# Kernel tuning notes

Hardware: AMD Instinct MI355X
Metric: run time of the kernel (lower is better)

Reference implementation:

```python
import jax, jax.numpy as jnp
import numpy as np

B, D, P, E, C = 2048, 4096, 64, 8, 64
K = D // P  # conv kernel = stride = input_dim / patch_num


def setup_inputs() -> dict:
    key = jax.random.key(0)
    k1, k2, k3, k4 = jax.random.split(key, 4)
    x = jax.random.normal(k1, (B, 1, D), jnp.float32)
    router_w = jax.random.normal(k2, (E, K), jnp.float32) * 0.02   # Router conv weight [E,1,K] squeezed
    expert_w = jax.random.normal(k3, (E, 2 * C, K), jnp.float32) * 0.001  # per-expert conv weights (small=True scaling)
    expert_b = jax.random.normal(k4, (E, 2 * C), jnp.float32) * 0.001
    return {"x": x, "router_w": router_w, "expert_w": expert_w, "expert_b": expert_b}


def reference(x, router_w, expert_w, expert_b):
    b, _, d = x.shape
    e, k = router_w.shape
    p = d // k
    c = expert_w.shape[1] // 2

    # Conv1d(1, ch, K, stride=K) == per-patch matmul; sum over dim 2 == sum over patches.
    patches = x.reshape(b, p, k)                                   # [B,P,K]

    # Router (eval mode: no noise)
    select = jnp.einsum('bpk,ek->be', patches, router_w)           # [B,E]

    # top1 routing
    gate = jnp.max(select, axis=-1)                                # [B]
    index = jnp.argmax(select, axis=-1)                            # [B]
    onehot = jax.nn.one_hot(index, e, dtype=select.dtype)          # [B,E]

    # aux load-balance loss
    density = onehot.mean(axis=0)
    density_proxy = select.mean(axis=0)
    loss = (density_proxy * density).mean() * float(e ** 2)

    # combine/dispatch (mask_flat is all ones for top1)
    combine = gate[:, None] * onehot                               # [B,E]
    dispatch = jax.lax.stop_gradient((combine != 0).astype(select.dtype))  # bool cast detaches grad
    select0 = dispatch

    # Dense dispatch: every expert sees the full batch, zero-masked by dispatch.
    # z[e,b,c,p] = conv of (dispatch[b,e]*x[b]) with expert e's kernel, + bias
    z = jnp.einsum('bpk,eck->ebcp', patches, expert_w)             # [E,B,2C,P]
    z = z * dispatch.T[:, :, None, None] + expert_b[:, None, :, None]
    z = z ** 3                                                     # nonlinear=True
    s = z.sum(axis=-1)                                             # sum over patches -> [E,B,2C]
    expert_out = jnp.stack([s[..., :c].sum(-1), s[..., c:].sum(-1)], axis=-1)  # [E,B,2]

    out = jnp.einsum('be,ebl->bl', combine, expert_out)            # [B,2]
    out = jax.nn.softmax(out, axis=1)
    return out, select0, loss
```

## Files before the change

### kernel.cpp

```cpp
#include <hip/hip_runtime.h>

#define BB 2048
#define DD 4096
#define PP 64
#define KK 64
#define EE 8
#define C2 128
#define NBLK BB
#define NGRP 32

typedef __attribute__((ext_vector_type(8))) short short8;
typedef __attribute__((ext_vector_type(4))) float floatx4;

__device__ float g_sum[NGRP][16] = {};

__device__ inline unsigned pack2_trunc(float lo, float hi) {
    unsigned ul = __builtin_bit_cast(unsigned, lo);
    unsigned uh = __builtin_bit_cast(unsigned, hi);
    return (uh & 0xFFFF0000u) | (ul >> 16);
}

__device__ inline void gload16(const float* src, float* lds_dst_uniform) {
    __builtin_amdgcn_global_load_lds(
        (const __attribute__((address_space(1))) unsigned int*)src,
        (__attribute__((address_space(3))) unsigned int*)lds_dst_uniform, 16, 0, 0);
}

__global__ __launch_bounds__(256) void moe_main(
    const float* __restrict__ x, const float* __restrict__ rw,
    const float* __restrict__ ew, const float* __restrict__ eb,
    float* __restrict__ out)
{
    __shared__ float xs[64 * 64];
    __shared__ float sh_d[4][8];
    __shared__ float sh_h[4];
    const int lane = threadIdx.x & 63;
    const int w = threadIdx.x >> 6;
    const int b = blockIdx.x;
    const int r = lane & 15, q = lane >> 4;
    const float* xb = x + (size_t)b * DD;

    #pragma unroll
    for (int j = 0; j < 4; ++j) {
        const int row = w * 16 + j * 4 + (lane >> 4);
        const int g   = (lane & 15) ^ (row & 7);
        gload16(xb + row * 64 + g * 4, &xs[(w * 16 + j * 4) * 64]);
    }
    asm volatile("s_waitcnt vmcnt(0)" ::: "memory");

    const int s = r & 7;
    float ps[16];
    #pragma unroll
    for (int kb = 0; kb < 2; ++kb) {
        const float* base = &xs[(w * 16 + r) * 64 + kb * 32];
        float4 v0 = *(const float4*)(base + (((q * 2 + 0) ^ s) << 2));
        float4 v1 = *(const float4*)(base + (((q * 2 + 1) ^ s) << 2));
        ps[kb*8+0] = v0.x; ps[kb*8+1] = v0.y; ps[kb*8+2] = v0.z; ps[kb*8+3] = v0.w;
        ps[kb*8+4] = v1.x; ps[kb*8+5] = v1.y; ps[kb*8+6] = v1.z; ps[kb*8+7] = v1.w;
    }

    #pragma unroll
    for (int e2 = 0; e2 < 8; ++e2) {
        const float* rwe = rw + e2 * KK;
        float4 a0 = *(const float4*)(rwe + q * 8);
        float4 a1 = *(const float4*)(rwe + q * 8 + 4);
        float4 b0 = *(const float4*)(rwe + 32 + q * 8);
        float4 b1 = *(const float4*)(rwe + 32 + q * 8 + 4);
        float t = ps[0]*a0.x + ps[1]*a0.y + ps[2]*a0.z + ps[3]*a0.w
                + ps[4]*a1.x + ps[5]*a1.y + ps[6]*a1.z + ps[7]*a1.w
                + ps[8]*b0.x + ps[9]*b0.y + ps[10]*b0.z + ps[11]*b0.w
                + ps[12]*b1.x + ps[13]*b1.y + ps[14]*b1.z + ps[15]*b1.w;
        t += __shfl_xor(t, 1);  t += __shfl_xor(t, 2);  t += __shfl_xor(t, 4);
        t += __shfl_xor(t, 8);  t += __shfl_xor(t, 16); t += __shfl_xor(t, 32);
        if (lane == 0) sh_d[w][e2] = t;
    }
    __syncthreads();

    float d[8];
    #pragma unroll
    for (int e2 = 0; e2 < 8; ++e2)
        d[e2] = ((sh_d[0][e2] + sh_d[1][e2]) + sh_d[2][e2]) + sh_d[3][e2];
    float gate = d[0]; int e = 0;
    #pragma unroll
    for (int e2 = 1; e2 < 8; ++e2)
        if (d[e2] > gate) { gate = d[e2]; e = e2; }

    if (w == 0 && lane < 8) {
        float on = (gate != 0.f) ? 1.f : 0.f;
        out[BB * 2 + b * 8 + lane] = (lane == e) ? on : 0.f;
        atomicAdd(&g_sum[b & (NGRP - 1)][lane], d[lane]);
        if (lane == e) atomicAdd(&g_sum[b & (NGRP - 1)][8 + lane], 1.f);
    }

    short8 af[8];
    #pragma unroll
    for (int mt = 0; mt < 4; ++mt) {
        #pragma unroll
        for (int kb = 0; kb < 2; ++kb) {
            const float* base = &xs[(mt * 16 + r) * 64 + kb * 32];
            float4 v0 = *(const float4*)(base + (((q * 2 + 0) ^ s) << 2));
            float4 v1 = *(const float4*)(base + (((q * 2 + 1) ^ s) << 2));
            uint4 u;
            u.x = pack2_trunc(v0.x, v0.y); u.y = pack2_trunc(v0.z, v0.w);
            u.z = pack2_trunc(v1.x, v1.y); u.w = pack2_trunc(v1.z, v1.w);
            af[mt * 2 + kb] = __builtin_bit_cast(short8, u);
        }
    }

    const float* we = ew + (size_t)e * (C2 * KK);
    float h = 0.f;
    #pragma unroll
    for (int ntl = 0; ntl < 2; ++ntl) {
        const int nt = w * 2 + ntl;
        float bs = eb[e * C2 + nt * 16 + r];
        const float* wr = we + (nt * 16 + r) * KK + q * 8;
        float4 w0 = *(const float4*)wr;
        float4 w1 = *(const float4*)(wr + 4);
        float4 w2 = *(const float4*)(wr + 32);
        float4 w3 = *(const float4*)(wr + 36);
        uint4 u0, u1;
        u0.x = pack2_trunc(w0.x, w0.y); u0.y = pack2_trunc(w0.z, w0.w);
        u0.z = pack2_trunc(w1.x, w1.y); u0.w = pack2_trunc(w1.z, w1.w);
        u1.x = pack2_trunc(w2.x, w2.y); u1.y = pack2_trunc(w2.z, w2.w);
        u1.z = pack2_trunc(w3.x, w3.y); u1.w = pack2_trunc(w3.z, w3.w);
        short8 bf0 = __builtin_bit_cast(short8, u0);
        short8 bf1 = __builtin_bit_cast(short8, u1);
        #pragma unroll
        for (int mt = 0; mt < 4; ++mt) {
            floatx4 a4 = (floatx4){0.f, 0.f, 0.f, 0.f};
            a4 = __builtin_amdgcn_mfma_f32_16x16x32_bf16(af[mt*2+0], bf0, a4, 0, 0, 0);
            a4 = __builtin_amdgcn_mfma_f32_16x16x32_bf16(af[mt*2+1], bf1, a4, 0, 0, 0);
            #pragma unroll
            for (int i = 0; i < 4; ++i) {
                float z = a4[i] + bs;
                h = fmaf(z * z, z, h);
            }
        }
    }
    #pragma unroll
    for (int off = 1; off < 64; off <<= 1)
        h += __shfl_xor(h, off);

    if (lane == 0) sh_h[w] = h;
    __syncthreads();

    if (threadIdx.x == 0) {
        float l0 = gate * (sh_h[0] + sh_h[1]);
        float l1 = gate * (sh_h[2] + sh_h[3]);
        float m = fmaxf(l0, l1);
        float e0 = __expf(l0 - m), e1 = __expf(l1 - m);
        float inv = 1.f / (e0 + e1);
        float2 o; o.x = e0 * inv; o.y = e1 * inv;
        *(float2*)(out + b * 2) = o;
    }
}

__global__ __launch_bounds__(256) void loss2(float* __restrict__ out)
{
    __shared__ float red[16][16];
    __shared__ float m[16];
    const int t = threadIdx.x;
    const int j = t & 15, k = t >> 4;

    float v = g_sum[k][j] + g_sum[k + 16][j];
    red[k][j] = v;
    __syncthreads();

    g_sum[k][j] = 0.f;
    g_sum[k + 16][j] = 0.f;

    if (t < 16) {
        float sv = 0.f;
        #pragma unroll
        for (int kk = 0; kk < 16; ++kk) sv += red[kk][t];
        m[t] = sv;
    }
    __syncthreads();
    if (t == 0) {
        float loss = 0.f;
        #pragma unroll
        for (int e2 = 0; e2 < 8; ++e2)
            loss += (m[e2] * (1.f / BB)) * (m[8 + e2] * (1.f / BB));
        out[BB * 2 + BB * 8] = loss * (float)EE;
    }
}

extern "C" void kernel_launch(void* const* d_in, const int* in_sizes, int n_in,
                              void* d_out, int out_size, void* d_ws, size_t ws_size,
                              hipStream_t stream) {
    (void)in_sizes; (void)n_in; (void)out_size; (void)d_ws; (void)ws_size;
    const float* x  = (const float*)d_in[0];
    const float* rw = (const float*)d_in[1];
    const float* ew = (const float*)d_in[2];
    const float* eb = (const float*)d_in[3];
    float* out = (float*)d_out;

    moe_main<<<NBLK, 256, 0, stream>>>(x, rw, ew, eb, out);
    loss2<<<1, 256, 0, stream>>>(out);
}
```

Before: 97.49 us.

## Split MFMA work by patch rows per wave instead of channel tiles, drop LDS staging

Each wave now owns its 16 patch rows and loops over all 8 channel tiles, instead of owning 2 channel tiles across all 64 patches. The activation fragment therefore comes straight from the same registers already loaded for the router, so the global-to-LDS staging and the LDS re-reads go away. In exchange, each wave loads the full expert weight slice (8 tiles instead of 2), which quadruples weight reads per block, though those are likely cache-resident. Output partials are kept per half and reduced across waves.

```diff
diff --git a/kernel.cpp b/kernel.cpp
--- a/kernel.cpp
+++ b/kernel.cpp
@@ -20,44 +20,26 @@
     return (uh & 0xFFFF0000u) | (ul >> 16);
 }
 
-__device__ inline void gload16(const float* src, float* lds_dst_uniform) {
-    __builtin_amdgcn_global_load_lds(
-        (const __attribute__((address_space(1))) unsigned int*)src,
-        (__attribute__((address_space(3))) unsigned int*)lds_dst_uniform, 16, 0, 0);
-}
-
 __global__ __launch_bounds__(256) void moe_main(
     const float* __restrict__ x, const float* __restrict__ rw,
     const float* __restrict__ ew, const float* __restrict__ eb,
     float* __restrict__ out)
 {
-    __shared__ float xs[64 * 64];
     __shared__ float sh_d[4][8];
-    __shared__ float sh_h[4];
+    __shared__ float sh_h[4][2];
     const int lane = threadIdx.x & 63;
     const int w = threadIdx.x >> 6;
     const int b = blockIdx.x;
     const int r = lane & 15, q = lane >> 4;
     const float* xb = x + (size_t)b * DD;
 
-    #pragma unroll
-    for (int j = 0; j < 4; ++j) {
-        const int row = w * 16 + j * 4 + (lane >> 4);
-        const int g   = (lane & 15) ^ (row & 7);
-        gload16(xb + row * 64 + g * 4, &xs[(w * 16 + j * 4) * 64]);
-    }
-    asm volatile("s_waitcnt vmcnt(0)" ::: "memory");
-
-    const int s = r & 7;
-    float ps[16];
-    #pragma unroll
-    for (int kb = 0; kb < 2; ++kb) {
-        const float* base = &xs[(w * 16 + r) * 64 + kb * 32];
-        float4 v0 = *(const float4*)(base + (((q * 2 + 0) ^ s) << 2));
-        float4 v1 = *(const float4*)(base + (((q * 2 + 1) ^ s) << 2));
-        ps[kb*8+0] = v0.x; ps[kb*8+1] = v0.y; ps[kb*8+2] = v0.z; ps[kb*8+3] = v0.w;
-        ps[kb*8+4] = v1.x; ps[kb*8+5] = v1.y; ps[kb*8+6] = v1.z; ps[kb*8+7] = v1.w;
-    }
+    const float* xbase = xb + (w * 16 + r) * 64;
+    float4 v0 = *(const float4*)(xbase + q * 8);
+    float4 v1 = *(const float4*)(xbase + q * 8 + 4);
+    float4 v2 = *(const float4*)(xbase + 32 + q * 8);
+    float4 v3 = *(const float4*)(xbase + 32 + q * 8 + 4);
+    float ps[16] = {v0.x, v0.y, v0.z, v0.w, v1.x, v1.y, v1.z, v1.w,
+                    v2.x, v2.y, v2.z, v2.w, v3.x, v3.y, v3.z, v3.w};
 
     #pragma unroll
     for (int e2 = 0; e2 < 8; ++e2) {
@@ -92,26 +74,18 @@
         if (lane == e) atomicAdd(&g_sum[b & (NGRP - 1)][8 + lane], 1.f);
     }
 
-    short8 af[8];
-    #pragma unroll
-    for (int mt = 0; mt < 4; ++mt) {
-        #pragma unroll
-        for (int kb = 0; kb < 2; ++kb) {
-            const float* base = &xs[(mt * 16 + r) * 64 + kb * 32];
-            float4 v0 = *(const float4*)(base + (((q * 2 + 0) ^ s) << 2));
-            float4 v1 = *(const float4*)(base + (((q * 2 + 1) ^ s) << 2));
-            uint4 u;
-            u.x = pack2_trunc(v0.x, v0.y); u.y = pack2_trunc(v0.z, v0.w);
-            u.z = pack2_trunc(v1.x, v1.y); u.w = pack2_trunc(v1.z, v1.w);
-            af[mt * 2 + kb] = __builtin_bit_cast(short8, u);
-        }
-    }
+    uint4 ua, ub;
+    ua.x = pack2_trunc(ps[0], ps[1]);  ua.y = pack2_trunc(ps[2],  ps[3]);
+    ua.z = pack2_trunc(ps[4], ps[5]);  ua.w = pack2_trunc(ps[6],  ps[7]);
+    ub.x = pack2_trunc(ps[8], ps[9]);  ub.y = pack2_trunc(ps[10], ps[11]);
+    ub.z = pack2_trunc(ps[12], ps[13]); ub.w = pack2_trunc(ps[14], ps[15]);
+    short8 af0 = __builtin_bit_cast(short8, ua);
+    short8 af1 = __builtin_bit_cast(short8, ub);
 
     const float* we = ew + (size_t)e * (C2 * KK);
-    float h = 0.f;
+    float h0 = 0.f, h1 = 0.f;
     #pragma unroll
-    for (int ntl = 0; ntl < 2; ++ntl) {
-        const int nt = w * 2 + ntl;
+    for (int nt = 0; nt < 8; ++nt) {
         float bs = eb[e * C2 + nt * 16 + r];
         const float* wr = we + (nt * 16 + r) * KK + q * 8;
         float4 w0 = *(const float4*)wr;
@@ -125,28 +99,29 @@
         u1.z = pack2_trunc(w3.x, w3.y); u1.w = pack2_trunc(w3.z, w3.w);
         short8 bf0 = __builtin_bit_cast(short8, u0);
         short8 bf1 = __builtin_bit_cast(short8, u1);
+        floatx4 a4 = (floatx4){0.f, 0.f, 0.f, 0.f};
+        a4 = __builtin_amdgcn_mfma_f32_16x16x32_bf16(af0, bf0, a4, 0, 0, 0);
+        a4 = __builtin_amdgcn_mfma_f32_16x16x32_bf16(af1, bf1, a4, 0, 0, 0);
+        float hh = 0.f;
         #pragma unroll
-        for (int mt = 0; mt < 4; ++mt) {
-            floatx4 a4 = (floatx4){0.f, 0.f, 0.f, 0.f};
-            a4 = __builtin_amdgcn_mfma_f32_16x16x32_bf16(af[mt*2+0], bf0, a4, 0, 0, 0);
-            a4 = __builtin_amdgcn_mfma_f32_16x16x32_bf16(af[mt*2+1], bf1, a4, 0, 0, 0);
-            #pragma unroll
-            for (int i = 0; i < 4; ++i) {
-                float z = a4[i] + bs;
-                h = fmaf(z * z, z, h);
-            }
+        for (int i = 0; i < 4; ++i) {
+            float z = a4[i] + bs;
+            hh = fmaf(z * z, z, hh);
         }
+        if (nt < 4) h0 += hh; else h1 += hh;
     }
     #pragma unroll
-    for (int off = 1; off < 64; off <<= 1)
-        h += __shfl_xor(h, off);
+    for (int off = 1; off < 64; off <<= 1) {
+        h0 += __shfl_xor(h0, off);
+        h1 += __shfl_xor(h1, off);
+    }
 
-    if (lane == 0) sh_h[w] = h;
+    if (lane == 0) { sh_h[w][0] = h0; sh_h[w][1] = h1; }
     __syncthreads();
 
     if (threadIdx.x == 0) {
-        float l0 = gate * (sh_h[0] + sh_h[1]);
-        float l1 = gate * (sh_h[2] + sh_h[3]);
+        float l0 = gate * (((sh_h[0][0] + sh_h[1][0]) + sh_h[2][0]) + sh_h[3][0]);
+        float l1 = gate * (((sh_h[0][1] + sh_h[1][1]) + sh_h[2][1]) + sh_h[3][1]);
         float m = fmaxf(l0, l1);
         float e0 = __expf(l0 - m), e1 = __expf(l1 - m);
         float inv = 1.f / (e0 + e1);
```

Result: slower. 116.5 us (+19.5%).
